# Kernel tuning notes

Measured on AMD Instinct MI355X. Metric: run time of the kernel, lower is better.

## Reference

```python
import jax, jax.numpy as jnp
import numpy as np

N_QUBITS = 6
N_LAYERS = 2
QSVT_DEGREE = 3
BATCH = 128
SEQ_LEN = 512
DIM = 2 ** N_QUBITS
# wire 0 is the most-significant bit in the statevector index (PennyLane convention)
_POP = np.array([bin(i).count('1') for i in range(DIM)], dtype=np.float32)
PHASE_SIGN = jnp.asarray(N_QUBITS - 2.0 * _POP)  # (DIM,): sum_w (1 - 2*bit_w)


def _rx(t):
    c = jnp.cos(0.5 * t).astype(jnp.complex64)
    s = (-1j * jnp.sin(0.5 * t)).astype(jnp.complex64)
    return jnp.stack([jnp.stack([c, s]), jnp.stack([s, c])])


def _ry(t):
    c = jnp.cos(0.5 * t).astype(jnp.complex64)
    s = jnp.sin(0.5 * t).astype(jnp.complex64)
    return jnp.stack([jnp.stack([c, -s]), jnp.stack([s, c])])


def _rz(t):
    e = jnp.exp(-0.5j * t.astype(jnp.complex64))
    z = jnp.zeros((), jnp.complex64)
    return jnp.stack([jnp.stack([e, z]), jnp.stack([z, jnp.conj(e)])])


def _apply_1q(psi, U, w):
    # psi: (B,) + (2,)*N_QUBITS ; U: (2,2) complex, same for all batch elems
    psi = jnp.moveaxis(psi, 1 + w, -1)
    psi = psi @ U.T
    return jnp.moveaxis(psi, -1, 1 + w)


def _apply_ry_batched(psi, theta, w):
    # RY with a per-batch angle theta: (B,)
    psi = jnp.moveaxis(psi, 1 + w, -1)
    c = jnp.cos(0.5 * theta).reshape((-1,) + (1,) * (N_QUBITS - 1))
    s = jnp.sin(0.5 * theta).reshape((-1,) + (1,) * (N_QUBITS - 1))
    a, b = psi[..., 0], psi[..., 1]
    psi = jnp.stack([c * a - s * b, s * a + c * b], axis=-1)
    return jnp.moveaxis(psi, -1, 1 + w)


def _cnot(psi, c, t):
    p0 = jax.lax.index_in_dim(psi, 0, axis=1 + c, keepdims=True)
    p1 = jax.lax.index_in_dim(psi, 1, axis=1 + c, keepdims=True)
    p1 = jnp.flip(p1, axis=1 + t)
    return jnp.concatenate([p0, p1], axis=1 + c)


def _circuit_step(h, x, params, poly):
    # h, x: (B, N_QUBITS) angles. Returns <Z_w> per qubit: (B, N_QUBITS).
    B = h.shape[0]
    # 1) state encoding: RY(h_w)|0> = cos(h/2)|0> + sin(h/2)|1>  (product state)
    c, s = jnp.cos(0.5 * h), jnp.sin(0.5 * h)
    psi = jnp.ones((B, 1), jnp.complex64)
    for w in range(N_QUBITS):
        amp = jnp.stack([c[:, w], s[:, w]], axis=-1).astype(jnp.complex64)  # (B,2)
        psi = (psi[:, :, None] * amp[:, None, :]).reshape(B, -1)
    psi = psi.reshape((B,) + (2,) * N_QUBITS)
    # 2) QSVT block: RZ(coeff*pi) on every wire fuses into one diagonal phase
    for d in range(QSVT_DEGREE + 1):
        theta = poly[d] * np.pi
        phase = jnp.exp((-0.5j) * theta * PHASE_SIGN)  # (DIM,)
        psi = (psi.reshape(B, -1) * phase[None, :]).reshape((B,) + (2,) * N_QUBITS)
        for i in range(N_QUBITS - 1):
            psi = _cnot(psi, i, i + 1)
        psi = _cnot(psi, N_QUBITS - 1, 0)  # ring closure
    # 3) variational layers: per-wire RZ@RY@RX (RX applied first), then CNOT chain
    idx = 0
    for _ in range(N_LAYERS):
        for i in range(N_QUBITS):
            U = _rz(params[idx + 2]) @ _ry(params[idx + 1]) @ _rx(params[idx])
            psi = _apply_1q(psi, U, i)
            idx += 3
        for i in range(N_QUBITS - 1):
            psi = _cnot(psi, i, i + 1)
    # 4) input injection: RY(x_w) with per-batch angles
    for w in range(N_QUBITS):
        psi = _apply_ry_batched(psi, x[:, w], w)
    # 5) measurement: <Z_w> = P(bit_w=0) - P(bit_w=1)
    p = jnp.abs(psi) ** 2
    zs = []
    for w in range(N_QUBITS):
        axes = tuple(a for a in range(1, N_QUBITS + 1) if a != 1 + w)
        pw = p.sum(axis=axes)  # (B,2)
        zs.append(pw[:, 0] - pw[:, 1])
    return jnp.stack(zs, axis=-1)


def _ssm_pass(angles, params, poly, reverse):
    a = jnp.flip(angles, axis=1) if reverse else angles
    xs = jnp.moveaxis(a, 1, 0)  # (T, B, n)
    h0 = jnp.zeros((a.shape[0], N_QUBITS), jnp.float32)

    def step(h, x):
        hn = _circuit_step(h, x, params, poly)
        return hn, hn

    _, ys = jax.lax.scan(step, h0, xs)
    out = jnp.moveaxis(ys, 0, 1)  # (B, T, n)
    return jnp.flip(out, axis=1) if reverse else out


def setup_inputs() -> dict:
    key = jax.random.key(0)
    k0, k1, k2, k3 = jax.random.split(key, 4)
    angles = jax.random.uniform(k0, (BATCH, SEQ_LEN, N_QUBITS), jnp.float32) * np.float32(np.pi)
    poly_coeffs = jax.random.normal(k1, (QSVT_DEGREE + 1,), jnp.float32) * 0.1
    fwd_params = jax.random.normal(k2, (N_QUBITS * N_LAYERS * 3,), jnp.float32) * 0.1
    bwd_params = jax.random.normal(k3, (N_QUBITS * N_LAYERS * 3,), jnp.float32) * 0.1
    fwd_coeff = jnp.full((1,), 0.5, jnp.float32)
    bwd_coeff = jnp.full((1,), 0.5, jnp.float32)
    return {'angles': angles, 'poly_coeffs': poly_coeffs, 'fwd_params': fwd_params,
            'bwd_params': bwd_params, 'fwd_coeff': fwd_coeff, 'bwd_coeff': bwd_coeff}


def reference(angles, poly_coeffs, fwd_params, bwd_params, fwd_coeff, bwd_coeff):
    h_fwd = _ssm_pass(angles, fwd_params, poly_coeffs, reverse=False)
    h_bwd = _ssm_pass(angles, bwd_params, poly_coeffs, reverse=True)
    return jax.nn.sigmoid(fwd_coeff) * h_fwd + jax.nn.sigmoid(bwd_coeff) * h_bwd
```

## Files before the change

kernel.cpp:

```cpp
#include <hip/hip_runtime.h>
#include <hip/hip_bf16.h>
#include <stdint.h>

#define BATCH 128
#define SEQ   512
#define NW    6
#define DIM   64
#define NELEM (BATCH * SEQ * NW)
#define PI_F  3.14159265358979323846f
#define NCONV 1536

typedef float v2f __attribute__((ext_vector_type(2)));

__device__ __forceinline__ v2f pkfma(float s, v2f m, v2f a) {
    return __builtin_elementwise_fma((v2f){s, s}, m, a);
}

template <int CTRL>
__device__ __forceinline__ void red_stage3(float v[3]) {
#pragma unroll
    for (int k = 0; k < 3; ++k)
        v[k] += __int_as_float(__builtin_amdgcn_update_dpp(
            0, __float_as_int(v[k]), CTRL, 0xF, 0xF, false));
}

__device__ __forceinline__ void sincos_half(float h, float& s, float& c) {
    const float u = h * h;
    c = fmaf(u, fmaf(u, 2.6041667e-3f, -0.125f), 1.0f);
    s = h * fmaf(u, fmaf(u, 2.6041667e-4f, -2.0833333e-2f), 0.5f);
}

__device__ __forceinline__ float ldf(const void* p, int i, bool bf) {
    if (bf) {
        uint32_t u = (uint32_t)((const uint16_t*)p)[i];
        return __uint_as_float(u << 16);
    }
    return ((const float*)p)[i];
}

__global__ void k_prep(const void* ang, const void* poly, const void* fp,
                       const void* bp, const void* fc, const void* bc,
                       float* __restrict__ cs, float* __restrict__ misc,
                       float* __restrict__ Mg, int* __restrict__ flag) {
    __shared__ int cnt;
    if (threadIdx.x == 0) cnt = 0;
    __syncthreads();
    {
        uint32_t w = ((const uint32_t*)ang)[threadIdx.x & 255];
        uint32_t e = (w >> 8) & 0xFFu;
        if (e >= 0x3Au && e <= 0x41u) atomicAdd(&cnt, 1);
    }
    __syncthreads();
    const bool bf = (cnt >= 128);

    if (blockIdx.x < NCONV) {
        const int i = blockIdx.x * 256 + threadIdx.x;
        if (i < NELEM) {
            float x = ldf(ang, i, bf);
            float s, c;
            __sincosf(x, &s, &c);
            cs[2 * i]     = c;
            cs[2 * i + 1] = s;
        }
        if (i == 200)      misc[76] = ldf(fc, 0, bf);
        else if (i == 201) misc[77] = ldf(bc, 0, bf);
        else if (i == 202) *flag = bf ? 1 : 0;
        return;
    }

    const int lane = threadIdx.x & 63;
    const int tix  = (blockIdx.x - NCONV) * 4 + (threadIdx.x >> 6);
    const int dir  = tix >> 6;
    const int col  = tix & 63;
    const void* prm = dir ? bp : fp;
    const int p = lane;

    float yr = (p == col) ? 1.f : 0.f;
    float yi = 0.f;

#pragma unroll
    for (int d = 0; d < 4; ++d) {
        const float th = 0.5f * PI_F * ldf(poly, d, bf) *
                         (float)(6 - 2 * (int)__popc((unsigned)p));
        float s, c;
        __sincosf(th, &s, &c);
        const float nr = yr * c + yi * s;
        const float ni = yi * c - yr * s;
        yr = nr; yi = ni;
#pragma unroll
        for (int k = 0; k < 6; ++k) {
            const int cw = k, tw = (k + 1) % 6;
            const int src = p ^ (((p >> (5 - cw)) & 1) << (5 - tw));
            yr = __shfl(yr, src, 64);
            yi = __shfl(yi, src, 64);
        }
    }

    int idx = 0;
#pragma unroll
    for (int l = 0; l < 2; ++l) {
#pragma unroll
        for (int w = 0; w < 6; ++w) {
            float cx, sx, cy, sy, cz, sz;
            __sincosf(0.5f * ldf(prm, idx + 0, bf), &sx, &cx);
            __sincosf(0.5f * ldf(prm, idx + 1, bf), &sy, &cy);
            __sincosf(0.5f * ldf(prm, idx + 2, bf), &sz, &cz);
            idx += 3;
            const float A = cy * cx, B = sy * sx, C = sy * cx, D = cy * sx;
            const float U00r = cz * A + sz * B, U00i = cz * B - sz * A;
            const float U11r = U00r,            U11i = sz * A - cz * B;
            const float Xr   = cz * C + sz * D, Xi   = sz * C - cz * D;
            const int m  = 1 << (5 - w);
            const int bb = (p >> (5 - w)) & 1;
            const float C1r = bb ? U11r : U00r;
            const float C1i = bb ? U11i : U00i;
            const float C2r = bb ? Xr : -Xr;
            const float C2i = Xi;
            const float pr = __shfl_xor(yr, m, 64);
            const float pi = __shfl_xor(yi, m, 64);
            const float nr = C1r * yr - C1i * yi + C2r * pr - C2i * pi;
            const float ni = C1r * yi + C1i * yr + C2r * pi + C2i * pr;
            yr = nr; yi = ni;
        }
#pragma unroll
        for (int k = 0; k < 5; ++k) {
            const int src = p ^ (((p >> (5 - k)) & 1) << (5 - (k + 1)));
            yr = __shfl(yr, src, 64);
            yi = __shfl(yi, src, 64);
        }
    }

    float* out = Mg + ((size_t)(dir * 64 + p) * 64 + (size_t)col) * 2;
    out[0] = yr;
    out[1] = yi;
}

__global__ void __launch_bounds__(256, 1) k_sim(const float* __restrict__ cs,
                                                const float* __restrict__ Mg,
                                                float* __restrict__ hbuf) {
    const int tid   = threadIdx.x;
    const int lane  = tid & 63;
    const int wv    = tid >> 6;
    const int chain = blockIdx.x;
    const int dir   = chain >> 7;
    const int b     = chain & 127;
    float* orow = hbuf + (size_t)dir * NELEM + (size_t)b * (SEQ * NW);
    const float* csrow = cs + (size_t)b * (SEQ * NW * 2);

    __shared__ __align__(16) float  cl[SEQ * 12];
    __shared__ __align__(16) float  zb[SEQ * NW];
    __shared__ float2 pY[2][4][DIM];
    __shared__ __align__(16) float  mR[12];

    {
        const float4* src = (const float4*)csrow;
        float4* dst = (float4*)cl;
#pragma unroll
        for (int k = 0; k < 6; ++k) {
            const int idx = tid + k * 256;
            dst[idx] = src[idx];
        }
    }

    v2f Mres[16];
    {
        const float2* mr2 =
            (const float2*)(Mg + (size_t)(dir * 64 + lane) * 128 + 32 * wv);
#pragma unroll
        for (int k = 0; k < 16; ++k) Mres[k] = (v2f){mr2[k].x, mr2[k].y};
    }

    const int w0  = (wv & 1) * 3;
    const int isX = wv >> 1;
    int zmask3[3], bpa3[3];
#pragma unroll
    for (int k = 0; k < 3; ++k) {
        const int w = w0 + k;
        zmask3[k] = ((lane >> (5 - w)) & 1) << 31;
        bpa3[k]   = (lane ^ (1 << (5 - w))) << 2;
    }
    const int ow0 = wv ^ 1, ow1 = wv ^ 2, ow2 = wv ^ 3;

    float h[6] = {0.f, 0.f, 0.f, 0.f, 0.f, 0.f};

    auto encode_matvec = [&](v2f& acc) {
        float cw6[6], sw6[6];
#pragma unroll
        for (int w = 0; w < 6; ++w) sincos_half(h[w], sw6[w], cw6[w]);
        const float t0 = (wv & 2) ? sw6[0] : cw6[0];
        const float t1 = (wv & 1) ? sw6[1] : cw6[1];
        const float A  = t0 * t1;
        float GH[4], GL[4];
        GH[0] = cw6[2] * cw6[3]; GH[1] = cw6[2] * sw6[3];
        GH[2] = sw6[2] * cw6[3]; GH[3] = sw6[2] * sw6[3];
#pragma unroll
        for (int a = 0; a < 4; ++a) GH[a] *= A;
        GL[0] = cw6[4] * cw6[5]; GL[1] = cw6[4] * sw6[5];
        GL[2] = sw6[4] * cw6[5]; GL[3] = sw6[4] * sw6[5];
        v2f y = {0.f, 0.f};
#pragma unroll
        for (int a = 0; a < 4; ++a) {
            v2f T = {0.f, 0.f};
#pragma unroll
            for (int b2 = 0; b2 < 4; ++b2)
                T = pkfma(GL[b2], Mres[4 * a + b2], T);
            y = pkfma(GH[a], T, y);
        }
        acc = y;
    };

    const float* cp = cl + (dir ? (SEQ - 1) * 12 : 0);
    const int   cstep = dir ? -12 : 12;
    float*       zp = zb + (dir ? (SEQ - 1) * NW : 0);
    const int   zstep = dir ? -NW : NW;

    __syncthreads();

    v2f myacc;
    encode_matvec(myacc);
    pY[0][wv][lane] = (float2){myacc.x, myacc.y};
    __syncthreads();

    for (int t = 0; t < SEQ; ++t) {
        const int buf = t & 1;

        const float2 yA = pY[buf][ow0][lane];
        const float2 yB = pY[buf][ow1][lane];
        const float2 yC = pY[buf][ow2][lane];
        const float4 xq0 = ((const float4*)cp)[0];
        const float4 xq1 = ((const float4*)cp)[1];
        const float4 xq2 = ((const float4*)cp)[2];
        cp += cstep;

        const float yr = (myacc.x + yA.x) + (yB.x + yC.x);
        const float yi = (myacc.y + yA.y) + (yB.y + yC.y);

        float v3[3];
        if (isX) {
            float pr[3], pi[3];
#pragma unroll
            for (int k = 0; k < 3; ++k)
                pr[k] = __int_as_float(
                    __builtin_amdgcn_ds_bpermute(bpa3[k], __float_as_int(yr)));
#pragma unroll
            for (int k = 0; k < 3; ++k)
                pi[k] = __int_as_float(
                    __builtin_amdgcn_ds_bpermute(bpa3[k], __float_as_int(yi)));
#pragma unroll
            for (int k = 0; k < 3; ++k) v3[k] = yr * pr[k] + yi * pi[k];
        } else {
            const float q = yr * yr + yi * yi;
#pragma unroll
            for (int k = 0; k < 3; ++k)
                v3[k] = __int_as_float(__float_as_int(q) ^ zmask3[k]);
        }
        red_stage3<0x111>(v3);
        red_stage3<0x112>(v3);
        red_stage3<0x114>(v3);
        red_stage3<0x118>(v3);
        red_stage3<0x142>(v3);
        red_stage3<0x143>(v3);

        if (lane == 63) {
            mR[wv * 3 + 0] = v3[0];
            mR[wv * 3 + 1] = v3[1];
            mR[wv * 3 + 2] = v3[2];
        }
        __syncthreads();

        const float4 m0 = ((const float4*)mR)[0];
        const float4 m1 = ((const float4*)mR)[1];
        const float4 m2 = ((const float4*)mR)[2];

        float z[6];
        z[0] = xq0.x * m0.x - xq0.y * m1.z;
        z[1] = xq0.z * m0.y - xq0.w * m1.w;
        z[2] = xq1.x * m0.z - xq1.y * m2.x;
        z[3] = xq1.z * m0.w - xq1.w * m2.y;
        z[4] = xq2.x * m1.x - xq2.y * m2.z;
        z[5] = xq2.z * m1.y - xq2.w * m2.w;

        if (tid == 63) {
#pragma unroll
            for (int w = 0; w < 6; ++w) zp[w] = z[w];
        }
        zp += zstep;
#pragma unroll
        for (int w = 0; w < 6; ++w) h[w] = z[w];

        encode_matvec(myacc);
        pY[buf ^ 1][wv][lane] = (float2){myacc.x, myacc.y};
        __syncthreads();
    }

    {
        const float4* zs4 = (const float4*)zb;
        float4* go = (float4*)orow;
#pragma unroll
        for (int k = 0; k < 3; ++k) {
            const int idx = tid + k * 256;
            go[idx] = zs4[idx];
        }
    }
}

__global__ void k_combine(const float* __restrict__ hbuf,
                          const float* __restrict__ misc,
                          void* __restrict__ out, const int* __restrict__ flag) {
    const int i = blockIdx.x * blockDim.x + threadIdx.x;
    if (i >= NELEM) return;
    const float sf = 1.f / (1.f + __expf(-misc[76]));
    const float sb = 1.f / (1.f + __expf(-misc[77]));
    const float v = sf * hbuf[i] + sb * hbuf[NELEM + i];
    if (*flag) ((__hip_bfloat16*)out)[i] = __float2bfloat16(v);
    else       ((float*)out)[i] = v;
}

extern "C" void kernel_launch(void* const* d_in, const int* in_sizes, int n_in,
                              void* d_out, int out_size, void* d_ws, size_t ws_size,
                              hipStream_t stream) {
    const void* ang  = d_in[0];
    const void* poly = d_in[1];
    const void* fp   = d_in[2];
    const void* bp   = d_in[3];
    const void* fc   = d_in[4];
    const void* bc   = d_in[5];

    float* cs   = (float*)d_ws + 32;
    float* misc = cs + 2 * NELEM;
    float* hbuf = misc + 128;
    float* Mg   = hbuf + 2 * NELEM;
    int*   flag = (int*)(Mg + 2 * 64 * 64 * 2);

    k_prep<<<NCONV + 32, 256, 0, stream>>>(ang, poly, fp, bp, fc, bc,
                                           cs, misc, Mg, flag);
    k_sim<<<256, 256, 0, stream>>>(cs, Mg, hbuf);
    k_combine<<<(NELEM + 255) / 256, 256, 0, stream>>>(hbuf, misc, d_out, flag);
}
```

Measured before the change: 346.4 us.

## Run each recurrence chain on a single wavefront and fuse angle sincos into sim

Each chain now runs on one 64-lane wavefront that holds the full 64x64 complex matrix in registers. This removes the four-wave split and the two block barriers per timestep, and the partner exchange uses swizzle, DPP and bpermute. The X and Z expectation terms are folded into one six-way DPP reduction, and readlane broadcasts the result without going through shared memory. The angle cos/sin conversion moves from the prep kernel into the sim kernel's load phase, which drops the intermediate workspace buffer. In exchange each lane does four times the matvec work serially and carries a large register footprint.

```diff
diff --git a/kernel.cpp b/kernel.cpp
--- a/kernel.cpp
+++ b/kernel.cpp
@@ -8,18 +8,18 @@
 #define DIM   64
 #define NELEM (BATCH * SEQ * NW)
 #define PI_F  3.14159265358979323846f
-#define NCONV 1536
 
 typedef float v2f __attribute__((ext_vector_type(2)));
+typedef uint16_t u16x8 __attribute__((ext_vector_type(8)));
 
 __device__ __forceinline__ v2f pkfma(float s, v2f m, v2f a) {
     return __builtin_elementwise_fma((v2f){s, s}, m, a);
 }
 
 template <int CTRL>
-__device__ __forceinline__ void red_stage3(float v[3]) {
-#pragma unroll
-    for (int k = 0; k < 3; ++k)
+__device__ __forceinline__ void red_stage6(float v[6]) {
+#pragma unroll
+    for (int k = 0; k < 6; ++k)
         v[k] += __int_as_float(__builtin_amdgcn_update_dpp(
             0, __float_as_int(v[k]), CTRL, 0xF, 0xF, false));
 }
@@ -40,8 +40,8 @@
 
 __global__ void k_prep(const void* ang, const void* poly, const void* fp,
                        const void* bp, const void* fc, const void* bc,
-                       float* __restrict__ cs, float* __restrict__ misc,
-                       float* __restrict__ Mg, int* __restrict__ flag) {
+                       float* __restrict__ misc, float* __restrict__ Mg,
+                       int* __restrict__ flag) {
     __shared__ int cnt;
     if (threadIdx.x == 0) cnt = 0;
     __syncthreads();
@@ -53,23 +53,15 @@
     __syncthreads();
     const bool bf = (cnt >= 128);
 
-    if (blockIdx.x < NCONV) {
-        const int i = blockIdx.x * 256 + threadIdx.x;
-        if (i < NELEM) {
-            float x = ldf(ang, i, bf);
-            float s, c;
-            __sincosf(x, &s, &c);
-            cs[2 * i]     = c;
-            cs[2 * i + 1] = s;
-        }
-        if (i == 200)      misc[76] = ldf(fc, 0, bf);
-        else if (i == 201) misc[77] = ldf(bc, 0, bf);
-        else if (i == 202) *flag = bf ? 1 : 0;
+    if (blockIdx.x == 32) {
+        if (threadIdx.x == 0)      misc[76] = ldf(fc, 0, bf);
+        else if (threadIdx.x == 1) misc[77] = ldf(bc, 0, bf);
+        else if (threadIdx.x == 2) *flag = bf ? 1 : 0;
         return;
     }
 
     const int lane = threadIdx.x & 63;
-    const int tix  = (blockIdx.x - NCONV) * 4 + (threadIdx.x >> 6);
+    const int tix  = blockIdx.x * 4 + (threadIdx.x >> 6);
     const int dir  = tix >> 6;
     const int col  = tix & 63;
     const void* prm = dir ? bp : fp;
@@ -135,170 +127,167 @@
     out[1] = yi;
 }
 
-__global__ void __launch_bounds__(256, 1) k_sim(const float* __restrict__ cs,
-                                                const float* __restrict__ Mg,
-                                                float* __restrict__ hbuf) {
-    const int tid   = threadIdx.x;
-    const int lane  = tid & 63;
-    const int wv    = tid >> 6;
+__global__ void __launch_bounds__(64, 1) k_sim(const void* __restrict__ ang,
+                                               const float* __restrict__ Mg,
+                                               float* __restrict__ hbuf,
+                                               const int* __restrict__ flag) {
+    const int lane  = threadIdx.x;
     const int chain = blockIdx.x;
     const int dir   = chain >> 7;
     const int b     = chain & 127;
-    float* orow = hbuf + (size_t)dir * NELEM + (size_t)b * (SEQ * NW);
-    const float* csrow = cs + (size_t)b * (SEQ * NW * 2);
-
-    __shared__ __align__(16) float  cl[SEQ * 12];
-    __shared__ __align__(16) float  zb[SEQ * NW];
-    __shared__ float2 pY[2][4][DIM];
-    __shared__ __align__(16) float  mR[12];
-
+    const bool bf   = (*flag != 0);
+
+    __shared__ __align__(16) float cl[SEQ * 12];
+    __shared__ __align__(16) float zb[SEQ * NW];
+
+    if (!bf) {
+        const float4* src =
+            (const float4*)((const float*)ang + (size_t)b * (SEQ * NW));
+#pragma unroll
+        for (int k = 0; k < 12; ++k) {
+            const int v = k * 64 + lane;
+            const float4 a = src[v];
+            __align__(16) float o[8];
+            float s, c;
+            __sincosf(a.x, &s, &c); o[0] = c; o[1] = s;
+            __sincosf(a.y, &s, &c); o[2] = c; o[3] = s;
+            __sincosf(a.z, &s, &c); o[4] = c; o[5] = s;
+            __sincosf(a.w, &s, &c); o[6] = c; o[7] = s;
+            ((float4*)cl)[2 * v]     = ((const float4*)o)[0];
+            ((float4*)cl)[2 * v + 1] = ((const float4*)o)[1];
+        }
+    } else {
+        const u16x8* src =
+            (const u16x8*)((const uint16_t*)ang + (size_t)b * (SEQ * NW));
+#pragma unroll
+        for (int k = 0; k < 6; ++k) {
+            const int v = k * 64 + lane;
+            const u16x8 a = src[v];
+            __align__(16) float o[16];
+#pragma unroll
+            for (int e = 0; e < 8; ++e) {
+                const float x = __uint_as_float(((uint32_t)a[e]) << 16);
+                float s, c;
+                __sincosf(x, &s, &c);
+                o[2 * e] = c; o[2 * e + 1] = s;
+            }
+#pragma unroll
+            for (int j = 0; j < 4; ++j)
+                ((float4*)cl)[4 * v + j] = ((const float4*)o)[j];
+        }
+    }
+
+    v2f Mc[64];
     {
-        const float4* src = (const float4*)csrow;
-        float4* dst = (float4*)cl;
-#pragma unroll
-        for (int k = 0; k < 6; ++k) {
-            const int idx = tid + k * 256;
-            dst[idx] = src[idx];
-        }
-    }
-
-    v2f Mres[16];
-    {
-        const float2* mr2 =
-            (const float2*)(Mg + (size_t)(dir * 64 + lane) * 128 + 32 * wv);
-#pragma unroll
-        for (int k = 0; k < 16; ++k) Mres[k] = (v2f){mr2[k].x, mr2[k].y};
-    }
-
-    const int w0  = (wv & 1) * 3;
-    const int isX = wv >> 1;
-    int zmask3[3], bpa3[3];
-#pragma unroll
-    for (int k = 0; k < 3; ++k) {
-        const int w = w0 + k;
-        zmask3[k] = ((lane >> (5 - w)) & 1) << 31;
-        bpa3[k]   = (lane ^ (1 << (5 - w))) << 2;
-    }
-    const int ow0 = wv ^ 1, ow1 = wv ^ 2, ow2 = wv ^ 3;
-
-    float h[6] = {0.f, 0.f, 0.f, 0.f, 0.f, 0.f};
-
-    auto encode_matvec = [&](v2f& acc) {
-        float cw6[6], sw6[6];
-#pragma unroll
-        for (int w = 0; w < 6; ++w) sincos_half(h[w], sw6[w], cw6[w]);
-        const float t0 = (wv & 2) ? sw6[0] : cw6[0];
-        const float t1 = (wv & 1) ? sw6[1] : cw6[1];
-        const float A  = t0 * t1;
-        float GH[4], GL[4];
-        GH[0] = cw6[2] * cw6[3]; GH[1] = cw6[2] * sw6[3];
-        GH[2] = sw6[2] * cw6[3]; GH[3] = sw6[2] * sw6[3];
-#pragma unroll
-        for (int a = 0; a < 4; ++a) GH[a] *= A;
-        GL[0] = cw6[4] * cw6[5]; GL[1] = cw6[4] * sw6[5];
-        GL[2] = sw6[4] * cw6[5]; GL[3] = sw6[4] * sw6[5];
-        v2f y = {0.f, 0.f};
-#pragma unroll
-        for (int a = 0; a < 4; ++a) {
-            v2f T = {0.f, 0.f};
-#pragma unroll
-            for (int b2 = 0; b2 < 4; ++b2)
-                T = pkfma(GL[b2], Mres[4 * a + b2], T);
-            y = pkfma(GH[a], T, y);
-        }
-        acc = y;
-    };
+        const float4* mr4 =
+            (const float4*)(Mg + (size_t)(dir * 64 + lane) * 128);
+#pragma unroll
+        for (int k = 0; k < 32; ++k) {
+            const float4 m = mr4[k];
+            Mc[2 * k]     = (v2f){m.x, m.y};
+            Mc[2 * k + 1] = (v2f){m.z, m.w};
+        }
+    }
+
+    int zmask[6];
+#pragma unroll
+    for (int w = 0; w < 6; ++w) zmask[w] = ((lane >> (5 - w)) & 1) << 31;
+    const int bpa0 = (lane ^ 32) << 2;
 
     const float* cp = cl + (dir ? (SEQ - 1) * 12 : 0);
     const int   cstep = dir ? -12 : 12;
     float*       zp = zb + (dir ? (SEQ - 1) * NW : 0);
     const int   zstep = dir ? -NW : NW;
 
+    float h[6] = {0.f, 0.f, 0.f, 0.f, 0.f, 0.f};
+
     __syncthreads();
 
-    v2f myacc;
-    encode_matvec(myacc);
-    pY[0][wv][lane] = (float2){myacc.x, myacc.y};
-    __syncthreads();
-
     for (int t = 0; t < SEQ; ++t) {
-        const int buf = t & 1;
-
-        const float2 yA = pY[buf][ow0][lane];
-        const float2 yB = pY[buf][ow1][lane];
-        const float2 yC = pY[buf][ow2][lane];
         const float4 xq0 = ((const float4*)cp)[0];
         const float4 xq1 = ((const float4*)cp)[1];
         const float4 xq2 = ((const float4*)cp)[2];
         cp += cstep;
 
-        const float yr = (myacc.x + yA.x) + (yB.x + yC.x);
-        const float yi = (myacc.y + yA.y) + (yB.y + yC.y);
-
-        float v3[3];
-        if (isX) {
-            float pr[3], pi[3];
-#pragma unroll
-            for (int k = 0; k < 3; ++k)
-                pr[k] = __int_as_float(
-                    __builtin_amdgcn_ds_bpermute(bpa3[k], __float_as_int(yr)));
-#pragma unroll
-            for (int k = 0; k < 3; ++k)
-                pi[k] = __int_as_float(
-                    __builtin_amdgcn_ds_bpermute(bpa3[k], __float_as_int(yi)));
-#pragma unroll
-            for (int k = 0; k < 3; ++k) v3[k] = yr * pr[k] + yi * pi[k];
-        } else {
-            const float q = yr * yr + yi * yi;
-#pragma unroll
-            for (int k = 0; k < 3; ++k)
-                v3[k] = __int_as_float(__float_as_int(q) ^ zmask3[k]);
-        }
-        red_stage3<0x111>(v3);
-        red_stage3<0x112>(v3);
-        red_stage3<0x114>(v3);
-        red_stage3<0x118>(v3);
-        red_stage3<0x142>(v3);
-        red_stage3<0x143>(v3);
+        float cw[6], sw[6];
+#pragma unroll
+        for (int w = 0; w < 6; ++w) sincos_half(h[w], sw[w], cw[w]);
+        float g01[4], g45[4], eH[8], eL[8];
+        g01[0] = cw[0] * cw[1]; g01[1] = cw[0] * sw[1];
+        g01[2] = sw[0] * cw[1]; g01[3] = sw[0] * sw[1];
+        g45[0] = cw[4] * cw[5]; g45[1] = cw[4] * sw[5];
+        g45[2] = sw[4] * cw[5]; g45[3] = sw[4] * sw[5];
+#pragma unroll
+        for (int j = 0; j < 8; ++j) {
+            eH[j] = g01[j >> 1] * ((j & 1) ? sw[2] : cw[2]);
+            eL[j] = ((j >> 2) ? sw[3] : cw[3]) * g45[j & 3];
+        }
+
+        v2f y = {0.f, 0.f};
+#pragma unroll
+        for (int jh = 0; jh < 8; ++jh) {
+            v2f n = {0.f, 0.f};
+#pragma unroll
+            for (int jl = 0; jl < 8; ++jl)
+                n = pkfma(eL[jl], Mc[8 * jh + jl], n);
+            y = pkfma(eH[jh], n, y);
+        }
+        const float yr = y.x, yi = y.y;
+        const int yri = __float_as_int(yr), yii = __float_as_int(yi);
+
+        float pr[6], pi[6];
+        pr[0] = __int_as_float(__builtin_amdgcn_ds_bpermute(bpa0, yri));
+        pi[0] = __int_as_float(__builtin_amdgcn_ds_bpermute(bpa0, yii));
+        pr[1] = __int_as_float(__builtin_amdgcn_ds_swizzle(yri, 0x401F));
+        pi[1] = __int_as_float(__builtin_amdgcn_ds_swizzle(yii, 0x401F));
+        pr[2] = __int_as_float(__builtin_amdgcn_ds_swizzle(yri, 0x201F));
+        pi[2] = __int_as_float(__builtin_amdgcn_ds_swizzle(yii, 0x201F));
+        pr[3] = __int_as_float(__builtin_amdgcn_ds_swizzle(yri, 0x101F));
+        pi[3] = __int_as_float(__builtin_amdgcn_ds_swizzle(yii, 0x101F));
+        pr[4] = __int_as_float(__builtin_amdgcn_update_dpp(0, yri, 0x4E, 0xF, 0xF, false));
+        pi[4] = __int_as_float(__builtin_amdgcn_update_dpp(0, yii, 0x4E, 0xF, 0xF, false));
+        pr[5] = __int_as_float(__builtin_amdgcn_update_dpp(0, yri, 0xB1, 0xF, 0xF, false));
+        pi[5] = __int_as_float(__builtin_amdgcn_update_dpp(0, yii, 0xB1, 0xF, 0xF, false));
+
+        const float q = fmaf(yr, yr, yi * yi);
+        const float cx[6] = {xq0.x, xq0.z, xq1.x, xq1.z, xq2.x, xq2.z};
+        const float sx[6] = {xq0.y, xq0.w, xq1.y, xq1.w, xq2.y, xq2.w};
+
+        float v[6];
+#pragma unroll
+        for (int w = 0; w < 6; ++w) {
+            const float cq  = __int_as_float(__float_as_int(cx[w] * q) ^ zmask[w]);
+            const float dot = fmaf(yr, pr[w], yi * pi[w]);
+            v[w] = fmaf(-sx[w], dot, cq);
+        }
+
+        red_stage6<0x111>(v);
+        red_stage6<0x112>(v);
+        red_stage6<0x114>(v);
+        red_stage6<0x118>(v);
+        red_stage6<0x142>(v);
+        red_stage6<0x143>(v);
 
         if (lane == 63) {
-            mR[wv * 3 + 0] = v3[0];
-            mR[wv * 3 + 1] = v3[1];
-            mR[wv * 3 + 2] = v3[2];
-        }
-        __syncthreads();
-
-        const float4 m0 = ((const float4*)mR)[0];
-        const float4 m1 = ((const float4*)mR)[1];
-        const float4 m2 = ((const float4*)mR)[2];
-
-        float z[6];
-        z[0] = xq0.x * m0.x - xq0.y * m1.z;
-        z[1] = xq0.z * m0.y - xq0.w * m1.w;
-        z[2] = xq1.x * m0.z - xq1.y * m2.x;
-        z[3] = xq1.z * m0.w - xq1.w * m2.y;
-        z[4] = xq2.x * m1.x - xq2.y * m2.z;
-        z[5] = xq2.z * m1.y - xq2.w * m2.w;
-
-        if (tid == 63) {
-#pragma unroll
-            for (int w = 0; w < 6; ++w) zp[w] = z[w];
+#pragma unroll
+            for (int w = 0; w < 6; ++w) zp[w] = v[w];
         }
         zp += zstep;
 #pragma unroll
-        for (int w = 0; w < 6; ++w) h[w] = z[w];
-
-        encode_matvec(myacc);
-        pY[buf ^ 1][wv][lane] = (float2){myacc.x, myacc.y};
-        __syncthreads();
-    }
+        for (int w = 0; w < 6; ++w)
+            h[w] = __int_as_float(
+                __builtin_amdgcn_readlane(__float_as_int(v[w]), 63));
+    }
+
+    __syncthreads();
 
     {
+        float* orow = hbuf + (size_t)dir * NELEM + (size_t)b * (SEQ * NW);
         const float4* zs4 = (const float4*)zb;
         float4* go = (float4*)orow;
 #pragma unroll
-        for (int k = 0; k < 3; ++k) {
-            const int idx = tid + k * 256;
+        for (int k = 0; k < 12; ++k) {
+            const int idx = k * 64 + lane;
             go[idx] = zs4[idx];
         }
     }
@@ -326,14 +315,12 @@
     const void* fc   = d_in[4];
     const void* bc   = d_in[5];
 
-    float* cs   = (float*)d_ws + 32;
-    float* misc = cs + 2 * NELEM;
+    float* misc = (float*)d_ws + 32;
     float* hbuf = misc + 128;
     float* Mg   = hbuf + 2 * NELEM;
     int*   flag = (int*)(Mg + 2 * 64 * 64 * 2);
 
-    k_prep<<<NCONV + 32, 256, 0, stream>>>(ang, poly, fp, bp, fc, bc,
-                                           cs, misc, Mg, flag);
-    k_sim<<<256, 256, 0, stream>>>(cs, Mg, hbuf);
+    k_prep<<<33, 256, 0, stream>>>(ang, poly, fp, bp, fc, bc, misc, Mg, flag);
+    k_sim<<<256, 64, 0, stream>>>(ang, Mg, hbuf, flag);
     k_combine<<<(NELEM + 255) / 256, 256, 0, stream>>>(hbuf, misc, d_out, flag);
 }
```

Measured after the change: 379.5 us. 1.1x slower.
